# Kernel optimization log

Hardware: AMD Instinct MI355X
Metric: run time of the kernel (lower is better)

## Reference

```python
import jax, jax.numpy as jnp
import numpy as np

B, L, S, D, V, H = 8, 1024, 1024, 256, 256, 8
HD = D // H   # traj head dim = 32
VD = V // H   # value head dim = 32
SCALE = HD ** -0.5

def _xavier(key, shape):
    fan_in, fan_out = shape[1], shape[0]
    std = (2.0 / (fan_in + fan_out)) ** 0.5
    return jax.random.normal(key, shape, dtype=jnp.float32) * std

def setup_inputs() -> dict:
    key = jax.random.key(0)
    ks = jax.random.split(key, 12)
    return {
        "q": jax.random.normal(ks[0], (B, L, D), dtype=jnp.float32),
        "k": jax.random.normal(ks[1], (B, S, D), dtype=jnp.float32),
        "v": jax.random.normal(ks[2], (B, S, D), dtype=jnp.float32),
        "q_identities": jax.random.randint(ks[3], (B, L), 0, 16),
        "k_identities": jax.random.randint(ks[4], (B, S), 0, 16),
        "mask": jnp.zeros((B, L, S), dtype=jnp.float32),
        "w_q_self": _xavier(ks[5], (D, D)),
        "w_q_other": _xavier(ks[6], (D, D)),
        "w_k_self": _xavier(ks[7], (D, D)),
        "w_k_other": _xavier(ks[8], (D, D)),
        "w_v": _xavier(ks[9], (V, D)),
        "fc_w": _xavier(ks[10], (V, V)),
        "fc_b": jnp.zeros((V,), dtype=jnp.float32),
    }

def _heads(x, hd):
    # [B, T, H*hd] -> [B, H, T, hd]
    Bc, T, _ = x.shape
    return x.reshape(Bc, T, H, hd).transpose(0, 2, 1, 3)

def reference(q, k, v, q_identities, k_identities, mask,
              w_q_self, w_q_other, w_k_self, w_k_other, w_v, fc_w, fc_b):
    # torch Linear: y = x @ W.T
    q_self = _heads(q @ w_q_self.T, HD) * SCALE   # [B,H,L,hd]
    q_other = _heads(q @ w_q_other.T, HD) * SCALE
    k_self = _heads(k @ w_k_self.T, HD)           # [B,H,S,hd]
    k_other = _heads(k @ w_k_other.T, HD)
    vh = _heads(v @ w_v.T, VD)                    # [B,H,S,vd]

    att_self = jnp.einsum('bhld,bhsd->bhls', q_self, k_self)
    att_other = jnp.einsum('bhld,bhsd->bhls', q_other, k_other)

    same = (q_identities[:, :, None] == k_identities[:, None, :])[:, None]  # [B,1,L,S]
    attention = jnp.where(same, att_self, att_other) + mask[:, None]
    attention = jax.nn.softmax(attention, axis=-1)  # [B,H,L,S]

    out = jnp.einsum('bhls,bhsd->bhld', attention, vh)     # [B,H,L,vd]
    out = out.transpose(0, 2, 1, 3).reshape(B, L, V)
    out = out @ fc_w.T + fc_b
    return out, attention.sum(axis=1) / H
```

## Files before the change

kernel.cpp:

```cpp
#include <hip/hip_runtime.h>
#include <hip/hip_bf16.h>

typedef float f32x4 __attribute__((ext_vector_type(4)));
typedef __bf16 bf16x8 __attribute__((ext_vector_type(8)));
typedef unsigned short us4 __attribute__((ext_vector_type(4)));

constexpr int B = 8, L = 1024, S = 1024, H = 8;
constexpr float SCALE = 0.17677669529663687f;

__device__ __forceinline__ unsigned short bfbits(float x) {
  return __builtin_bit_cast(unsigned short, (__bf16)x);
}
__device__ __forceinline__ unsigned int pk2(float a, float b) {
  return ((unsigned int)bfbits(b) << 16) | (unsigned int)bfbits(a);
}
__device__ __forceinline__ float unpk_lo(unsigned int u) {
  return __builtin_bit_cast(float, u << 16);
}
__device__ __forceinline__ float unpk_hi(unsigned int u) {
  return __builtin_bit_cast(float, u & 0xffff0000u);
}

__global__ __launch_bounds__(256) void proj_kernel(
    const float* __restrict__ q, const float* __restrict__ k, const float* __restrict__ v,
    const float* __restrict__ wqs, const float* __restrict__ wqo,
    const float* __restrict__ wks, const float* __restrict__ wko,
    const float* __restrict__ wv,
    __bf16* __restrict__ qs, __bf16* __restrict__ qo,
    __bf16* __restrict__ ksl, __bf16* __restrict__ kol,
    __bf16* __restrict__ vht)
{
  const int proj = blockIdx.z;
  const float* X; const float* W;
  if (proj == 0)      { X = q; W = wqs; }
  else if (proj == 1) { X = q; W = wqo; }
  else if (proj == 2) { X = k; W = wks; }
  else if (proj == 3) { X = k; W = wko; }
  else                { X = v; W = wv;  }

  __shared__ __align__(16) char smem[2 * 64 * 264 * 2];
  __bf16 (*At)[264] = (__bf16(*)[264])smem;
  __bf16 (*Wt)[264] = (__bf16(*)[264])(smem + 64 * 264 * 2);
  float  (*ct)[65]  = (float(*)[65])smem;

  const int tid = threadIdx.x;
  const int m0 = blockIdx.y * 64, n0 = blockIdx.x * 64;

  for (int i = tid; i < 4096; i += 256) {
    int row = i >> 6, c4 = (i & 63) << 2;
    float4 a  = *reinterpret_cast<const float4*>(X + (size_t)(m0 + row) * 256 + c4);
    float4 ww = *reinterpret_cast<const float4*>(W + (size_t)(n0 + row) * 256 + c4);
    us4 ap, wp;
    ap[0] = bfbits(a.x);  ap[1] = bfbits(a.y);  ap[2] = bfbits(a.z);  ap[3] = bfbits(a.w);
    wp[0] = bfbits(ww.x); wp[1] = bfbits(ww.y); wp[2] = bfbits(ww.z); wp[3] = bfbits(ww.w);
    *reinterpret_cast<us4*>(&At[row][c4]) = ap;
    *reinterpret_cast<us4*>(&Wt[row][c4]) = wp;
  }
  __syncthreads();

  const int w = tid >> 6, lane = tid & 63;
  const int cl = lane & 15, g = lane >> 4;

  f32x4 zf = {0.f, 0.f, 0.f, 0.f};
  f32x4 acc[4] = {zf, zf, zf, zf};
  #pragma unroll
  for (int kk = 0; kk < 8; ++kk) {
    bf16x8 af = *reinterpret_cast<const bf16x8*>(&At[w * 16 + cl][kk * 32 + g * 8]);
    #pragma unroll
    for (int nt = 0; nt < 4; ++nt) {
      bf16x8 bfr = *reinterpret_cast<const bf16x8*>(&Wt[nt * 16 + cl][kk * 32 + g * 8]);
      acc[nt] = __builtin_amdgcn_mfma_f32_16x16x32_bf16(af, bfr, acc[nt], 0, 0, 0);
    }
  }
  if (proj < 2) {
    #pragma unroll
    for (int nt = 0; nt < 4; ++nt)
      #pragma unroll
      for (int r = 0; r < 4; ++r) acc[nt][r] *= SCALE;
  }

  if (proj < 4) {
    __bf16* Y = (proj == 0) ? qs : (proj == 1) ? qo : (proj == 2) ? ksl : kol;
    #pragma unroll
    for (int nt = 0; nt < 4; ++nt) {
      int n = n0 + nt * 16 + cl;
      int h = n >> 5, hd = n & 31;
      #pragma unroll
      for (int r = 0; r < 4; ++r) {
        int m = m0 + w * 16 + g * 4 + r;
        int bb = m >> 10, t = m & 1023;
        Y[(((size_t)(bb * H + h)) * 1024 + t) * 32 + hd] = (__bf16)acc[nt][r];
      }
    }
  } else {
    __syncthreads();
    #pragma unroll
    for (int nt = 0; nt < 4; ++nt)
      #pragma unroll
      for (int r = 0; r < 4; ++r)
        ct[w * 16 + g * 4 + r][nt * 16 + cl] = acc[nt][r];
    __syncthreads();
    int n_local = tid >> 2;
    int sc = (tid & 3) << 4;
    int n = n0 + n_local;
    int h = n >> 5, vd = n & 31;
    int bb = m0 >> 10;
    int sbase = m0 & 1023;
    int t32 = (sbase + sc) >> 5, off = (sbase + sc) & 31;
    __bf16* dst = vht + ((((size_t)(bb * H + h)) * 32 + t32)) * 1024 + vd * 32 + off;
    bf16x8 o0, o1;
    #pragma unroll
    for (int j = 0; j < 8; ++j) o0[j] = (__bf16)ct[sc + j][n_local];
    #pragma unroll
    for (int j = 0; j < 8; ++j) o1[j] = (__bf16)ct[sc + 8 + j][n_local];
    *reinterpret_cast<bf16x8*>(dst) = o0;
    *reinterpret_cast<bf16x8*>(dst + 8) = o1;
  }
}

__global__ __launch_bounds__(256) void attn_kernel(
    const __bf16* __restrict__ qs, const __bf16* __restrict__ qo,
    const __bf16* __restrict__ ksl, const __bf16* __restrict__ kol,
    const __bf16* __restrict__ vht,
    const int* __restrict__ qid, const int* __restrict__ kid,
    const float* __restrict__ mask,
    float* __restrict__ out_part, __bf16* __restrict__ att_part)
{
  const int b = blockIdx.y;
  const int l0 = blockIdx.x * 16;
  const int hg = blockIdx.z;
  const int tid = threadIdx.x;
  const int w = tid >> 6, lane = tid & 63;
  const int cl = lane & 15, g = lane >> 4;
  const int sw = w * 256;

  __shared__ __align__(16) __bf16 pbuf[4][16][264];
  __shared__ float redsum[2][4][16];

  int qid_r[4];
  #pragma unroll
  for (int r = 0; r < 4; ++r) qid_r[r] = qid[b * L + l0 + g * 4 + r];
  int kid_st[16];
  #pragma unroll
  for (int st = 0; st < 16; ++st) kid_st[st] = kid[b * S + sw + st * 16 + cl];

  unsigned int mreg[16][2];
  {
    const float* mrow = mask + ((size_t)b * L + l0 + g * 4) * S + sw + cl;
    #pragma unroll
    for (int st = 0; st < 16; ++st) {
      float a0 = mrow[(size_t)0 * S + st * 16];
      float a1 = mrow[(size_t)1 * S + st * 16];
      float a2 = mrow[(size_t)2 * S + st * 16];
      float a3 = mrow[(size_t)3 * S + st * 16];
      mreg[st][0] = pk2(a0, a1);
      mreg[st][1] = pk2(a2, a3);
    }
  }

  f32x4 zf = {0.f, 0.f, 0.f, 0.f};
  float att_acc[8][8];
  #pragma unroll
  for (int kt = 0; kt < 8; ++kt)
    #pragma unroll
    for (int j = 0; j < 8; ++j) att_acc[kt][j] = 0.f;

  const size_t PSZ = (size_t)B * L * 256;

  for (int hi = 0; hi < 4; ++hi) {
    const int h = hg * 4 + hi;
    const int par = hi & 1;
    const size_t hb = ((size_t)(b * H + h)) * 1024;

    bf16x8 qsf = *reinterpret_cast<const bf16x8*>(qs + (hb + l0 + cl) * 32 + g * 8);
    bf16x8 qof = *reinterpret_cast<const bf16x8*>(qo + (hb + l0 + cl) * 32 + g * 8);
    const __bf16* kb1 = ksl + (hb + sw) * 32;
    const __bf16* kb2 = kol + (hb + sw) * 32;

    float rsum[4] = {0.f, 0.f, 0.f, 0.f};
    #pragma unroll
    for (int st = 0; st < 16; ++st) {
      bf16x8 kf1 = *reinterpret_cast<const bf16x8*>(kb1 + st * 512 + cl * 32 + g * 8);
      bf16x8 kf2 = *reinterpret_cast<const bf16x8*>(kb2 + st * 512 + cl * 32 + g * 8);
      f32x4 as = __builtin_amdgcn_mfma_f32_16x16x32_bf16(qsf, kf1, zf, 0, 0, 0);
      f32x4 ao = __builtin_amdgcn_mfma_f32_16x16x32_bf16(qof, kf2, zf, 0, 0, 0);
      int kc = kid_st[st];
      float mv[4] = {unpk_lo(mreg[st][0]), unpk_hi(mreg[st][0]),
                     unpk_lo(mreg[st][1]), unpk_hi(mreg[st][1])};
      #pragma unroll
      for (int r = 0; r < 4; ++r) {
        float lg = ((qid_r[r] == kc) ? as[r] : ao[r]) + mv[r];
        float p = __expf(fminf(lg, 60.f));
        pbuf[w][g * 4 + r][st * 16 + cl] = (__bf16)p;
        rsum[r] += p;
      }
    }

    #pragma unroll
    for (int r = 0; r < 4; ++r) {
      float sv = rsum[r];
      sv += __shfl_xor(sv, 1); sv += __shfl_xor(sv, 2);
      sv += __shfl_xor(sv, 4); sv += __shfl_xor(sv, 8);
      rsum[r] = sv;
    }
    if (cl == 0) {
      #pragma unroll
      for (int r = 0; r < 4; ++r) redsum[par][w][g * 4 + r] = rsum[r];
    }
    __syncthreads();
    float zrow = redsum[par][0][cl] + redsum[par][1][cl] +
                 redsum[par][2][cl] + redsum[par][3][cl];
    float inv_cl = 1.0f / zrow;
    float invq[4];
    #pragma unroll
    for (int r = 0; r < 4; ++r) invq[r] = __shfl(inv_cl, g * 4 + r);

    f32x4 oa0 = zf, oa1 = zf;
    const __bf16* vb = vht + ((size_t)(b * H + h)) * 32 * 1024 + (size_t)w * 8 * 1024;
    #pragma unroll
    for (int kt = 0; kt < 8; ++kt) {
      bf16x8 pa = *reinterpret_cast<const bf16x8*>(&pbuf[w][cl][kt * 32 + g * 8]);
      #pragma unroll
      for (int j = 0; j < 8; ++j) att_acc[kt][j] += (float)pa[j] * inv_cl;
      bf16x8 v0 = *reinterpret_cast<const bf16x8*>(vb + kt * 1024 + cl * 32 + g * 8);
      bf16x8 v1 = *reinterpret_cast<const bf16x8*>(vb + kt * 1024 + 512 + cl * 32 + g * 8);
      oa0 = __builtin_amdgcn_mfma_f32_16x16x32_bf16(pa, v0, oa0, 0, 0, 0);
      oa1 = __builtin_amdgcn_mfma_f32_16x16x32_bf16(pa, v1, oa1, 0, 0, 0);
    }
    float* op = out_part + (size_t)w * PSZ + ((size_t)(b * 1024 + l0)) * 256 + h * 32;
    #pragma unroll
    for (int r = 0; r < 4; ++r) {
      op[(size_t)(g * 4 + r) * 256 + cl]      = oa0[r] * invq[r];
      op[(size_t)(g * 4 + r) * 256 + cl + 16] = oa1[r] * invq[r];
    }
  }

  __bf16* ap = att_part + (size_t)hg * ((size_t)B * L * S) +
               ((size_t)(b * 1024 + l0 + cl)) * 1024 + sw + g * 8;
  #pragma unroll
  for (int kt = 0; kt < 8; ++kt) {
    bf16x8 o;
    #pragma unroll
    for (int j = 0; j < 8; ++j) o[j] = (__bf16)(att_acc[kt][j] * 0.125f);
    *reinterpret_cast<bf16x8*>(ap + kt * 32) = o;
  }
}

__global__ __launch_bounds__(256) void fc_kernel(
    const float* __restrict__ part, const float* __restrict__ fcw,
    const float* __restrict__ fcb, float* __restrict__ out)
{
  __shared__ __align__(16) __bf16 At[64][264];
  __shared__ __align__(16) __bf16 Wt[64][264];
  const int tid = threadIdx.x;
  const int m0 = blockIdx.y * 64, n0 = blockIdx.x * 64;
  const size_t PSZ = (size_t)B * L * 256;

  for (int i = tid; i < 4096; i += 256) {
    int row = i >> 6, c4 = (i & 63) << 2;
    size_t off = (size_t)(m0 + row) * 256 + c4;
    float4 s0 = *reinterpret_cast<const float4*>(part + off);
    float4 s1 = *reinterpret_cast<const float4*>(part + PSZ + off);
    float4 s2 = *reinterpret_cast<const float4*>(part + 2 * PSZ + off);
    float4 s3 = *reinterpret_cast<const float4*>(part + 3 * PSZ + off);
    float4 ww = *reinterpret_cast<const float4*>(fcw + (size_t)(n0 + row) * 256 + c4);
    us4 ap, wp;
    ap[0] = bfbits(s0.x + s1.x + s2.x + s3.x);
    ap[1] = bfbits(s0.y + s1.y + s2.y + s3.y);
    ap[2] = bfbits(s0.z + s1.z + s2.z + s3.z);
    ap[3] = bfbits(s0.w + s1.w + s2.w + s3.w);
    wp[0] = bfbits(ww.x); wp[1] = bfbits(ww.y); wp[2] = bfbits(ww.z); wp[3] = bfbits(ww.w);
    *reinterpret_cast<us4*>(&At[row][c4]) = ap;
    *reinterpret_cast<us4*>(&Wt[row][c4]) = wp;
  }
  __syncthreads();

  const int w = tid >> 6, lane = tid & 63;
  const int cl = lane & 15, g = lane >> 4;
  f32x4 zf = {0.f, 0.f, 0.f, 0.f};
  f32x4 acc[4] = {zf, zf, zf, zf};
  #pragma unroll
  for (int kk = 0; kk < 8; ++kk) {
    bf16x8 af = *reinterpret_cast<const bf16x8*>(&At[w * 16 + cl][kk * 32 + g * 8]);
    #pragma unroll
    for (int nt = 0; nt < 4; ++nt) {
      bf16x8 bfr = *reinterpret_cast<const bf16x8*>(&Wt[nt * 16 + cl][kk * 32 + g * 8]);
      acc[nt] = __builtin_amdgcn_mfma_f32_16x16x32_bf16(af, bfr, acc[nt], 0, 0, 0);
    }
  }
  #pragma unroll
  for (int nt = 0; nt < 4; ++nt) {
    int n = n0 + nt * 16 + cl;
    float bias = fcb[n];
    #pragma unroll
    for (int r = 0; r < 4; ++r)
      out[(size_t)(m0 + w * 16 + g * 4 + r) * 256 + n] = acc[nt][r] + bias;
  }
}

__global__ __launch_bounds__(256) void reduce_att_kernel(
    const __bf16* __restrict__ ap, float* __restrict__ am)
{
  const size_t APSZ = (size_t)B * L * S;
  size_t i = ((size_t)blockIdx.x * 256 + threadIdx.x) * 8;
  bf16x8 a = *reinterpret_cast<const bf16x8*>(ap + i);
  bf16x8 c = *reinterpret_cast<const bf16x8*>(ap + APSZ + i);
  float4 o0, o1;
  o0.x = (float)a[0] + (float)c[0]; o0.y = (float)a[1] + (float)c[1];
  o0.z = (float)a[2] + (float)c[2]; o0.w = (float)a[3] + (float)c[3];
  o1.x = (float)a[4] + (float)c[4]; o1.y = (float)a[5] + (float)c[5];
  o1.z = (float)a[6] + (float)c[6]; o1.w = (float)a[7] + (float)c[7];
  *reinterpret_cast<float4*>(am + i) = o0;
  *reinterpret_cast<float4*>(am + i + 4) = o1;
}

extern "C" void kernel_launch(void* const* d_in, const int* in_sizes, int n_in,
                              void* d_out, int out_size, void* d_ws, size_t ws_size,
                              hipStream_t stream) {
  const float* q    = (const float*)d_in[0];
  const float* k    = (const float*)d_in[1];
  const float* v    = (const float*)d_in[2];
  const int*   qid  = (const int*)d_in[3];
  const int*   kid  = (const int*)d_in[4];
  const float* mask = (const float*)d_in[5];
  const float* wqs  = (const float*)d_in[6];
  const float* wqo  = (const float*)d_in[7];
  const float* wks  = (const float*)d_in[8];
  const float* wko  = (const float*)d_in[9];
  const float* wv   = (const float*)d_in[10];
  const float* fcw  = (const float*)d_in[11];
  const float* fcb  = (const float*)d_in[12];

  char* ws = (char*)d_ws;
  const size_t ACT = (size_t)B * L * 256 * sizeof(__bf16);
  __bf16* qs  = (__bf16*)(ws + 0 * ACT);
  __bf16* qo  = (__bf16*)(ws + 1 * ACT);
  __bf16* ksl = (__bf16*)(ws + 2 * ACT);
  __bf16* kol = (__bf16*)(ws + 3 * ACT);
  __bf16* vht = (__bf16*)(ws + 4 * ACT);
  float*  out_part = (float*)(ws + 5 * ACT);
  __bf16* att_part = (__bf16*)(ws + 5 * ACT + 4 * (size_t)B * L * 256 * 4);

  float* out0 = (float*)d_out;
  float* att_mean = out0 + (size_t)B * L * 256;

  proj_kernel<<<dim3(4, 128, 5), 256, 0, stream>>>(q, k, v, wqs, wqo, wks, wko, wv,
                                                   qs, qo, ksl, kol, vht);
  attn_kernel<<<dim3(64, 8, 2), 256, 0, stream>>>(qs, qo, ksl, kol, vht, qid, kid, mask,
                                                  out_part, att_part);
  fc_kernel<<<dim3(4, 128), 256, 0, stream>>>(out_part, fcw, fcb, out0);
  reduce_att_kernel<<<dim3(4096), 256, 0, stream>>>(att_part, att_mean);
}
```

Baseline: 261.0 us.

## Split attention heads across more blocks, pretranspose mask to bf16, use exp2

The attention grid grows from 2 to 4 head groups, so each block now handles 2 heads instead of 4. This doubles the block count for better occupancy, but the partial attention buffer grows to four slices that the reduce kernel must sum. A new prep kernel converts the fp32 mask into a bf16 transposed tile layout, already scaled by log2e, so attention blocks can load it with vector reads instead of strided scalar loads. The q scale folds in log2e so the softmax can use native exp2. The cost is an extra pass over the mask and more partial-buffer traffic; the hidden parts of attn_kernel must index partials by the new hg range for this to be consistent.

```diff
diff --git a/kernel.cpp b/kernel.cpp
--- a/kernel.cpp
+++ b/kernel.cpp
@@ -6,19 +6,35 @@
 typedef unsigned short us4 __attribute__((ext_vector_type(4)));
 
 constexpr int B = 8, L = 1024, S = 1024, H = 8;
-constexpr float SCALE = 0.17677669529663687f;
+constexpr float LOG2E = 1.4426950408889634f;
+constexpr float SCALE_Q = 0.17677669529663687f * 1.4426950408889634f;
 
 __device__ __forceinline__ unsigned short bfbits(float x) {
   return __builtin_bit_cast(unsigned short, (__bf16)x);
 }
-__device__ __forceinline__ unsigned int pk2(float a, float b) {
-  return ((unsigned int)bfbits(b) << 16) | (unsigned int)bfbits(a);
-}
-__device__ __forceinline__ float unpk_lo(unsigned int u) {
-  return __builtin_bit_cast(float, u << 16);
-}
-__device__ __forceinline__ float unpk_hi(unsigned int u) {
-  return __builtin_bit_cast(float, u & 0xffff0000u);
+__device__ __forceinline__ float b2f(unsigned short u) {
+  return __builtin_bit_cast(float, (unsigned int)u << 16);
+}
+
+__global__ __launch_bounds__(256) void prep_mask_kernel(
+    const float* __restrict__ mask, __bf16* __restrict__ maskT)
+{
+  __shared__ float tile[16][65];
+  const int tid = threadIdx.x;
+  const int sc = blockIdx.x, lt = blockIdx.y, b = blockIdx.z;
+  const int s0 = sc * 64;
+  const int q = tid >> 6, sl = tid & 63;
+  #pragma unroll
+  for (int rr = 0; rr < 4; ++rr) {
+    int row = q * 4 + rr;
+    tile[row][sl] = mask[((size_t)(b * 1024 + lt * 16 + row)) * 1024 + s0 + sl] * LOG2E;
+  }
+  __syncthreads();
+  const int sl2 = tid >> 2, rq = (tid & 3) * 4;
+  us4 o;
+  #pragma unroll
+  for (int j = 0; j < 4; ++j) o[j] = bfbits(tile[rq + j][sl2]);
+  *reinterpret_cast<us4*>(maskT + (((size_t)(b * 64 + lt)) * 1024 + s0 + sl2) * 16 + rq) = o;
 }
 
 __global__ __launch_bounds__(256) void proj_kernel(
@@ -76,7 +92,7 @@
     #pragma unroll
     for (int nt = 0; nt < 4; ++nt)
       #pragma unroll
-      for (int r = 0; r < 4; ++r) acc[nt][r] *= SCALE;
+      for (int r = 0; r < 4; ++r) acc[nt][r] *= SCALE_Q;
   }
 
   if (proj < 4) {
@@ -123,11 +139,12 @@
     const __bf16* __restrict__ ksl, const __bf16* __restrict__ kol,
     const __bf16* __restrict__ vht,
     const int* __restrict__ qid, const int* __restrict__ kid,
-    const float* __restrict__ mask,
+    const __bf16* __restrict__ maskT,
     float* __restrict__ out_part, __bf16* __restrict__ att_part)
 {
   const int b = blockIdx.y;
-  const int l0 = blockIdx.x * 16;
+  const int lt = blockIdx.x;
+  const int l0 = lt * 16;
   const int hg = blockIdx.z;
   const int tid = threadIdx.x;
   const int w = tid >> 6, lane = tid & 63;
@@ -144,18 +161,12 @@
   #pragma unroll
   for (int st = 0; st < 16; ++st) kid_st[st] = kid[b * S + sw + st * 16 + cl];
 
-  unsigned int mreg[16][2];
+  us4 mreg[16];
   {
-    const float* mrow = mask + ((size_t)b * L + l0 + g * 4) * S + sw + cl;
-    #pragma unroll
-    for (int st = 0; st < 16; ++st) {
-      float a0 = mrow[(size_t)0 * S + st * 16];
-      float a1 = mrow[(size_t)1 * S + st * 16];
-      float a2 = mrow[(size_t)2 * S + st * 16];
-      float a3 = mrow[(size_t)3 * S + st * 16];
-      mreg[st][0] = pk2(a0, a1);
-      mreg[st][1] = pk2(a2, a3);
-    }
+    const __bf16* mbase = maskT + ((size_t)(b * 64 + lt)) * 16384 + (size_t)(sw + cl) * 16 + g * 4;
+    #pragma unroll
+    for (int st = 0; st < 16; ++st)
+      mreg[st] = *reinterpret_cast<const us4*>(mbase + st * 256);
   }
 
   f32x4 zf = {0.f, 0.f, 0.f, 0.f};
@@ -167,9 +178,9 @@
 
   const size_t PSZ = (size_t)B * L * 256;
 
-  for (int hi = 0; hi < 4; ++hi) {
-    const int h = hg * 4 + hi;
-    const int par = hi & 1;
+  for (int hi = 0; hi < 2; ++hi) {
+    const int h = hg * 2 + hi;
+    const int par = hi;
     const size_t hb = ((size_t)(b * H + h)) * 1024;
 
     bf16x8 qsf = *reinterpret_cast<const bf16x8*>(qs + (hb + l0 + cl) * 32 + g * 8);
@@ -185,12 +196,10 @@
       f32x4 as = __builtin_amdgcn_mfma_f32_16x16x32_bf16(qsf, kf1, zf, 0, 0, 0);
       f32x4 ao = __builtin_amdgcn_mfma_f32_16x16x32_bf16(qof, kf2, zf, 0, 0, 0);
       int kc = kid_st[st];
-      float mv[4] = {unpk_lo(mreg[st][0]), unpk_hi(mreg[st][0]),
-                     unpk_lo(mreg[st][1]), unpk_hi(mreg[st][1])};
       #pragma unroll
       for (int r = 0; r < 4; ++r) {
-        float lg = ((qid_r[r] == kc) ? as[r] : ao[r]) + mv[r];
-        float p = __expf(fminf(lg, 60.f));
+        float lg = ((qid_r[r] == kc) ? as[r] : ao[r]) + b2f(mreg[st][r]);
+        float p = __builtin_amdgcn_exp2f(fminf(lg, 86.0f));
         pbuf[w][g * 4 + r][st * 16 + cl] = (__bf16)p;
         rsum[r] += p;
       }
@@ -305,11 +314,17 @@
   size_t i = ((size_t)blockIdx.x * 256 + threadIdx.x) * 8;
   bf16x8 a = *reinterpret_cast<const bf16x8*>(ap + i);
   bf16x8 c = *reinterpret_cast<const bf16x8*>(ap + APSZ + i);
+  bf16x8 d = *reinterpret_cast<const bf16x8*>(ap + 2 * APSZ + i);
+  bf16x8 e = *reinterpret_cast<const bf16x8*>(ap + 3 * APSZ + i);
   float4 o0, o1;
-  o0.x = (float)a[0] + (float)c[0]; o0.y = (float)a[1] + (float)c[1];
-  o0.z = (float)a[2] + (float)c[2]; o0.w = (float)a[3] + (float)c[3];
-  o1.x = (float)a[4] + (float)c[4]; o1.y = (float)a[5] + (float)c[5];
-  o1.z = (float)a[6] + (float)c[6]; o1.w = (float)a[7] + (float)c[7];
+  o0.x = ((float)a[0] + (float)c[0]) + ((float)d[0] + (float)e[0]);
+  o0.y = ((float)a[1] + (float)c[1]) + ((float)d[1] + (float)e[1]);
+  o0.z = ((float)a[2] + (float)c[2]) + ((float)d[2] + (float)e[2]);
+  o0.w = ((float)a[3] + (float)c[3]) + ((float)d[3] + (float)e[3]);
+  o1.x = ((float)a[4] + (float)c[4]) + ((float)d[4] + (float)e[4]);
+  o1.y = ((float)a[5] + (float)c[5]) + ((float)d[5] + (float)e[5]);
+  o1.z = ((float)a[6] + (float)c[6]) + ((float)d[6] + (float)e[6]);
+  o1.w = ((float)a[7] + (float)c[7]) + ((float)d[7] + (float)e[7]);
   *reinterpret_cast<float4*>(am + i) = o0;
   *reinterpret_cast<float4*>(am + i + 4) = o1;
 }
@@ -332,21 +347,25 @@
   const float* fcb  = (const float*)d_in[12];
 
   char* ws = (char*)d_ws;
-  const size_t ACT = (size_t)B * L * 256 * sizeof(__bf16);
+  const size_t ACT  = (size_t)B * L * 256 * sizeof(__bf16);
+  const size_t PSZB = (size_t)B * L * 256 * sizeof(float);
+  const size_t APSZB = (size_t)B * L * S * sizeof(__bf16);
   __bf16* qs  = (__bf16*)(ws + 0 * ACT);
   __bf16* qo  = (__bf16*)(ws + 1 * ACT);
   __bf16* ksl = (__bf16*)(ws + 2 * ACT);
   __bf16* kol = (__bf16*)(ws + 3 * ACT);
   __bf16* vht = (__bf16*)(ws + 4 * ACT);
   float*  out_part = (float*)(ws + 5 * ACT);
-  __bf16* att_part = (__bf16*)(ws + 5 * ACT + 4 * (size_t)B * L * 256 * 4);
+  __bf16* att_part = (__bf16*)(ws + 5 * ACT + 4 * PSZB);
+  __bf16* maskT    = (__bf16*)(ws + 5 * ACT + 4 * PSZB + 4 * APSZB);
 
   float* out0 = (float*)d_out;
   float* att_mean = out0 + (size_t)B * L * 256;
 
+  prep_mask_kernel<<<dim3(16, 64, 8), 256, 0, stream>>>(mask, maskT);
   proj_kernel<<<dim3(4, 128, 5), 256, 0, stream>>>(q, k, v, wqs, wqo, wks, wko, wv,
                                                    qs, qo, ksl, kol, vht);
-  attn_kernel<<<dim3(64, 8, 2), 256, 0, stream>>>(qs, qo, ksl, kol, vht, qid, kid, mask,
+  attn_kernel<<<dim3(64, 8, 4), 256, 0, stream>>>(qs, qo, ksl, kol, vht, qid, kid, maskT,
                                                   out_part, att_part);
   fc_kernel<<<dim3(4, 128), 256, 0, stream>>>(out_part, fcw, fcb, out0);
   reduce_att_kernel<<<dim3(4096), 256, 0, stream>>>(att_part, att_mean);
```

Measured after the change: 288.8 us. +10.7%, slower.
